# Kernel tuning notes

Hardware: AMD Instinct MI355X
Metric: run time of the kernel (lower is better)

Reference implementation:

```python
import jax, jax.numpy as jnp
import numpy as np

NODE_SIZE = 100000
DIM = 512
B = 2048
GAMMA = 3.0
LAMB = 20.0
TAU = 8.0


def setup_inputs() -> dict:
    key = jax.random.key(0)
    k1, k2 = jax.random.split(key)
    pairs = jax.random.randint(k1, (B, 2), 0, NODE_SIZE, dtype=jnp.int64 if jax.config.jax_enable_x64 else jnp.int32)
    emb = jax.random.normal(k2, (NODE_SIZE, DIM), dtype=jnp.float32)
    return {"pairs": pairs, "emb": emb}


def _align_loss(pairs, emb):
    l = pairs[:, 0]
    r = pairs[:, 1]
    l_emb = emb[l]                     # [B, D]
    r_emb = emb[r]                     # [B, D]
    pos_dis = jnp.sum(jnp.square(l_emb - r_emb), axis=-1, keepdims=True)  # [B, 1]

    emb_sq = jnp.sum(jnp.square(emb), axis=1)          # [N]

    def squared_dist(A):
        # ||a||^2 + ||b||^2 - 2 a.b  -> [B, N]
        a_sq = jnp.sum(jnp.square(A), axis=1, keepdims=True)
        return a_sq + emb_sq[None, :] - 2.0 * (A @ emb.T)

    l_neg_dis = squared_dist(l_emb)
    r_neg_dis = squared_dist(r_emb)

    # mask = 1 - one_hot(l) - one_hot(r), built without materializing one-hots
    rows = jnp.arange(B)
    mask = jnp.ones((B, NODE_SIZE), dtype=emb.dtype)
    mask = mask.at[rows, l].add(-1.0)
    mask = mask.at[rows, r].add(-1.0)

    def norm_lse(loss):
        loss = loss * mask
        mu = jax.lax.stop_gradient(jnp.mean(loss, axis=-1, keepdims=True))
        sd = jax.lax.stop_gradient(jnp.std(loss, axis=-1, keepdims=True))  # unbiased=False
        loss = (loss - mu) / sd
        return jax.scipy.special.logsumexp(LAMB * loss + TAU, axis=-1)

    l_loss = norm_lse(pos_dis - l_neg_dis + GAMMA)
    r_loss = norm_lse(pos_dis - r_neg_dis + GAMMA)
    return jnp.mean(l_loss + r_loss)


def reference(pairs, emb):
    return _align_loss(pairs, emb)
```

## Files before the change

### kernel.cpp

```cpp
#include <hip/hip_runtime.h>
#include <stdint.h>

#define NODES   100000
#define NPAD    100096
#define DIM     512
#define NPAIR   2048
#define MROWS   4096
#define NB      782
#define MPAGES  32
#define GAMMA_F 3.0f
#define LAMB_F  20.0f
#define TAU_F   8.0f
#define SHIFT_F 140.0f

#define TM 128
#define TN 128
#define BK 64

typedef __attribute__((ext_vector_type(8))) short          short8;
typedef __attribute__((ext_vector_type(8))) unsigned short ushort8;
typedef __attribute__((ext_vector_type(4))) float          f32x4;


__device__ __forceinline__ unsigned short f2bf(float f) {
    unsigned u = __float_as_uint(f);
    u += 0x7FFFu + ((u >> 16) & 1u);
    return (unsigned short)(u >> 16);
}
__device__ __forceinline__ float bf2f(unsigned short h) {
    return __uint_as_float(((unsigned)h) << 16);
}

__device__ __forceinline__ void gload_lds16(const void* g, void* l) {
    unsigned lofs = (unsigned)__builtin_amdgcn_readfirstlane((unsigned)(uintptr_t)l);
    auto lp = reinterpret_cast<__attribute__((address_space(3))) unsigned*>(lofs);
    auto gp = (const __attribute__((address_space(1))) unsigned*)g;
    __builtin_amdgcn_global_load_lds(gp, lp, 16, 0, 0);
}


__global__ void convert_stats_kernel(const float* __restrict__ emb,
                                     unsigned short* __restrict__ Ebf,
                                     float* __restrict__ esq,
                                     float* __restrict__ Spart,
                                     float* __restrict__ Tpart,
                                     float* __restrict__ E1part,
                                     float* __restrict__ E2part) {
    __shared__ float Sl[4][512];
    __shared__ float Tl[4][512];
    __shared__ float ew[8];
    const int b = blockIdx.x, t = threadIdx.x;
    const int lane = t & 63, wave = t >> 6;
    const int r0 = b * 196;
    float sacc[8], tacc[8];
    #pragma unroll
    for (int k = 0; k < 8; ++k) { sacc[k] = 0.f; tacc[k] = 0.f; }
    float e1 = 0.f, e2 = 0.f;
    for (int i = 0; i < 49; ++i) {
        const int row = r0 + i * 4 + wave;
        if (row >= NPAD) continue;
        const bool real = row < NODES;
        float v[8];
        float ss = 0.f;
        if (real) {
            const float4* p = (const float4*)(emb + (size_t)row * DIM + lane * 8);
            float4 a = p[0], bb = p[1];
            v[0]=a.x; v[1]=a.y; v[2]=a.z; v[3]=a.w;
            v[4]=bb.x; v[5]=bb.y; v[6]=bb.z; v[7]=bb.w;
            #pragma unroll
            for (int k = 0; k < 8; ++k) ss += v[k] * v[k];
        } else {
            #pragma unroll
            for (int k = 0; k < 8; ++k) v[k] = 0.f;
        }
        #pragma unroll
        for (int o = 1; o < 64; o <<= 1) ss += __shfl_xor(ss, o);
        ushort8 o8;
        float vr[8];
        #pragma unroll
        for (int k = 0; k < 8; ++k) { o8[k] = f2bf(v[k]); vr[k] = bf2f(o8[k]); }
        *(ushort8*)(Ebf + (size_t)row * DIM + lane * 8) = o8;
        if (lane == 0) esq[row] = ss;
        if (real) {
            #pragma unroll
            for (int k = 0; k < 8; ++k) { sacc[k] += vr[k]; tacc[k] += ss * vr[k]; }
            if (lane == 0) { e1 += ss; e2 += ss * ss; }
        }
    }
    #pragma unroll
    for (int k = 0; k < 8; ++k) {
        Sl[wave][lane * 8 + k] = sacc[k];
        Tl[wave][lane * 8 + k] = tacc[k];
    }
    if (lane == 0) { ew[wave] = e1; ew[4 + wave] = e2; }
    __syncthreads();
    #pragma unroll
    for (int kk = 0; kk < 2; ++kk) {
        const int d = 2 * t + kk;
        Spart[(size_t)b * 512 + d] = Sl[0][d] + Sl[1][d] + Sl[2][d] + Sl[3][d];
        Tpart[(size_t)b * 512 + d] = Tl[0][d] + Tl[1][d] + Tl[2][d] + Tl[3][d];
    }
    if (t == 0) E1part[b] = ew[0] + ew[1] + ew[2] + ew[3];
    if (t == 1) E2part[b] = ew[4] + ew[5] + ew[6] + ew[7];
}

__global__ void stats_merge_kernel(const float* __restrict__ Spart,
                                   const float* __restrict__ Tpart,
                                   const float* __restrict__ E1part,
                                   const float* __restrict__ E2part,
                                   float* __restrict__ Svec,
                                   float* __restrict__ Tvec,
                                   double* __restrict__ E12) {
    const int t = threadIdx.x;
    if (t < 512) {
        float s = 0.f;
        for (int b = 0; b < 512; ++b) s += Spart[(size_t)b * 512 + t];
        Svec[t] = s;
    } else {
        const int d = t - 512;
        float s = 0.f;
        for (int b = 0; b < 512; ++b) s += Tpart[(size_t)b * 512 + d];
        Tvec[d] = s;
    }
    if (t == 0) { double a = 0.0; for (int b = 0; b < 512; ++b) a += (double)E1part[b]; E12[0] = a; }
    if (t == 1) { double a = 0.0; for (int b = 0; b < 512; ++b) a += (double)E2part[b]; E12[1] = a; }
}

__global__ void gather_kernel(const int* __restrict__ pairs,
                              const float* __restrict__ emb,
                              unsigned short* __restrict__ Abf,
                              float* __restrict__ cvec,
                              float* __restrict__ posv) {
    const int p    = blockIdx.x;
    const int lane = threadIdx.x;
    const int li = pairs[2 * p], ri = pairs[2 * p + 1];
    const float4* pl = (const float4*)(emb + (size_t)li * DIM + lane * 8);
    const float4* pr = (const float4*)(emb + (size_t)ri * DIM + lane * 8);
    float4 a0 = pl[0], a1 = pl[1];
    float4 b0 = pr[0], b1 = pr[1];
    float la[8] = {a0.x,a0.y,a0.z,a0.w,a1.x,a1.y,a1.z,a1.w};
    float lb[8] = {b0.x,b0.y,b0.z,b0.w,b1.x,b1.y,b1.z,b1.w};
    float sa = 0.f, sb = 0.f, sd = 0.f;
    ushort8 oa, ob;
    #pragma unroll
    for (int i = 0; i < 8; ++i) {
        sa += la[i] * la[i];
        sb += lb[i] * lb[i];
        float d = la[i] - lb[i];
        sd += d * d;
        oa[i] = f2bf(la[i]);
        ob[i] = f2bf(lb[i]);
    }
    *(ushort8*)(Abf + (size_t)p * DIM + lane * 8)            = oa;
    *(ushort8*)(Abf + (size_t)(NPAIR + p) * DIM + lane * 8)  = ob;
    #pragma unroll
    for (int off = 1; off < 64; off <<= 1) {
        sa += __shfl_xor(sa, off);
        sb += __shfl_xor(sb, off);
        sd += __shfl_xor(sd, off);
    }
    if (lane == 0) {
        cvec[p]         = sd - sa + GAMMA_F;
        cvec[NPAIR + p] = sd - sb + GAMMA_F;
        posv[p]         = sd;
    }
}


__launch_bounds__(256, 2)
__global__ void gram_kernel(const unsigned short* __restrict__ Ebf,
                            float* __restrict__ Gpart) {
    __shared__ unsigned short ldsA[64 * 128];
    __shared__ unsigned short ldsB[64 * 128];
    const int tid  = threadIdx.x;
    const int lane = tid & 63;
    const int wave = tid >> 6;
    const int wx = wave & 1, wy = wave >> 1;
    const int d1base = blockIdx.y * 128;
    const int d2base = blockIdx.x * 128;
    const int bz = blockIdx.z;
    const int r15 = lane & 15, q = lane >> 4;

    f32x4 zero4 = {0.f, 0.f, 0.f, 0.f};
    f32x4 acc[4][4];
    #pragma unroll
    for (int i = 0; i < 4; ++i)
        #pragma unroll
        for (int j = 0; j < 4; ++j) acc[i][j] = zero4;

    for (int jc = bz; jc < NPAD / 64; jc += 32) {
        const int j0 = jc * 64;
        #pragma unroll
        for (int ii = 0; ii < 4; ++ii) {
            const int iss = wave * 4 + ii;
            const int row = iss * 4 + (lane >> 4);
            gload_lds16(Ebf + (size_t)(j0 + row) * DIM + d1base + (lane & 15) * 8,
                        &ldsA[iss * 4 * 128]);
            gload_lds16(Ebf + (size_t)(j0 + row) * DIM + d2base + (lane & 15) * 8,
                        &ldsB[iss * 4 * 128]);
        }
        __builtin_amdgcn_s_waitcnt(0);
        __syncthreads();
        #pragma unroll
        for (int h = 0; h < 2; ++h) {
            short8 af[4], bfv[4];
            #pragma unroll
            for (int mt = 0; mt < 4; ++mt) {
                const int m = wy * 64 + mt * 16 + r15;
                #pragma unroll
                for (int i = 0; i < 8; ++i)
                    af[mt][i] = (short)ldsA[(h * 32 + q * 8 + i) * 128 + m];
            }
            #pragma unroll
            for (int nt = 0; nt < 4; ++nt) {
                const int n = wx * 64 + nt * 16 + r15;
                #pragma unroll
                for (int i = 0; i < 8; ++i)
                    bfv[nt][i] = (short)ldsB[(h * 32 + q * 8 + i) * 128 + n];
            }
            #pragma unroll
            for (int mt = 0; mt < 4; ++mt)
                #pragma unroll
                for (int nt = 0; nt < 4; ++nt)
                    acc[mt][nt] = __builtin_amdgcn_mfma_f32_16x16x32_bf16(
                        af[mt], bfv[nt], acc[mt][nt], 0, 0, 0);
        }
        __syncthreads();
    }
    float* gp = Gpart + (size_t)bz * 512 * 512;
    #pragma unroll
    for (int mt = 0; mt < 4; ++mt)
        #pragma unroll
        for (int r = 0; r < 4; ++r) {
            const int d1 = d1base + wy * 64 + mt * 16 + q * 4 + r;
            #pragma unroll
            for (int nt = 0; nt < 4; ++nt) {
                const int d2 = d2base + wx * 64 + nt * 16 + r15;
                gp[d1 * 512 + d2] = acc[mt][nt][r];
            }
        }
}

__global__ void gram_merge_kernel(const float* __restrict__ Gpart,
                                  float* __restrict__ G) {
    const int idx = blockIdx.x * 256 + threadIdx.x;
    float s = 0.f;
    for (int b = 0; b < 32; ++b) s += Gpart[(size_t)b * 512 * 512 + idx];
    G[idx] = s;
}


__launch_bounds__(256)
__global__ void gu_kernel(const unsigned short* __restrict__ Abf,
                          const float* __restrict__ G,
                          const float* __restrict__ Svec,
                          const float* __restrict__ Tvec,
                          const double* __restrict__ E12,
                          const float* __restrict__ cvec,
                          const float* __restrict__ posv,
                          const int* __restrict__ pairs,
                          float* __restrict__ alpha_v,
                          float* __restrict__ shift_v) {
    __shared__ float u[8][512];
    __shared__ float red[8][3][4];
    const int t = threadIdx.x;
    const int lane = t & 63, wave = t >> 6;
    const int r0 = blockIdx.x * 8;
    #pragma unroll
    for (int p = 0; p < 8; ++p) {
        unsigned pk = *(const unsigned*)(Abf + (size_t)(r0 + p) * DIM + 2 * t);
        u[p][2 * t]     = bf2f((unsigned short)(pk & 0xffffu));
        u[p][2 * t + 1] = bf2f((unsigned short)(pk >> 16));
    }
    __syncthreads();
    float acc0[8], acc1[8];
    #pragma unroll
    for (int p = 0; p < 8; ++p) { acc0[p] = 0.f; acc1[p] = 0.f; }
    for (int d1 = 0; d1 < 512; ++d1) {
        const float2 g = *(const float2*)(G + d1 * 512 + 2 * t);
        #pragma unroll
        for (int p = 0; p < 8; ++p) {
            const float up = u[p][d1];
            acc0[p] += up * g.x;
            acc1[p] += up * g.y;
        }
    }
    const float sv0 = Svec[2 * t], sv1 = Svec[2 * t + 1];
    const float tv0 = Tvec[2 * t], tv1 = Tvec[2 * t + 1];
    #pragma unroll
    for (int p = 0; p < 8; ++p) {
        const float u0 = u[p][2 * t], u1 = u[p][2 * t + 1];
        float pdS = u0 * sv0 + u1 * sv1;
        float pdT = u0 * tv0 + u1 * tv1;
        float pq  = u0 * acc0[p] + u1 * acc1[p];
        #pragma unroll
        for (int off = 1; off < 64; off <<= 1) {
            pdS += __shfl_xor(pdS, off);
            pdT += __shfl_xor(pdT, off);
            pq  += __shfl_xor(pq,  off);
        }
        if (lane == 0) {
            red[p][0][wave] = pdS;
            red[p][1][wave] = pdT;
            red[p][2][wave] = pq;
        }
    }
    __syncthreads();
    if (t < 8) {
        const int p = t;
        const double dS = (double)red[p][0][0] + red[p][0][1] + red[p][0][2] + red[p][0][3];
        const double dT = (double)red[p][1][0] + red[p][1][1] + red[p][1][2] + red[p][1][3];
        const double qq = (double)red[p][2][0] + red[p][2][1] + red[p][2][2] + red[p][2][3];
        const int row = r0 + p;
        const int pp  = row & (NPAIR - 1);
        const double c  = (double)cvec[row];
        const double E1 = E12[0], E2 = E12[1];
        const double N  = (double)NODES;
        double Sx  = N * c + 2.0 * dS - E1;
        double Sxx = (N * c * c - 2.0 * c * E1 + E2) + 4.0 * (c * dS - dT) + 4.0 * qq;
        const int li = pairs[2 * pp], ri = pairs[2 * pp + 1];
        const double pos = (double)posv[pp];
        if (li != ri) {
            const double x1 = pos + (double)GAMMA_F, x2 = (double)GAMMA_F;
            Sx  -= x1 + x2;
            Sxx -= x1 * x1 + x2 * x2;
        } else {
            Sx -= 2.0 * (double)GAMMA_F;
        }
        const double mu  = Sx / N;
        const double var = Sxx / N - mu * mu;
        const double sd  = sqrt(fmax(var, 1e-30));
        const double al  = (double)LAMB_F / sd;
        alpha_v[row] = (float)al;
        shift_v[row] = (float)(al * mu + (double)SHIFT_F);
    }
}


__launch_bounds__(256, 2)
__global__ void gemm_kernel(const unsigned short* __restrict__ Abf,
                            const unsigned short* __restrict__ Ebf,
                            const float* __restrict__ cvec,
                            const float* __restrict__ esq,
                            const int*   __restrict__ pairs,
                            const float* __restrict__ alpha_v,
                            const float* __restrict__ shift_v,
                            float* __restrict__ psum) {
    __shared__ unsigned short ldsA[TM * BK];
    __shared__ unsigned short ldsB[TN * BK];
    __shared__ float red_s[2][TM];
    __shared__ float alsh[TM], csh[TM], cmsh[TM];
    __shared__ int   lish[TM], rish[TM];

    const int tid  = threadIdx.x;
    const int lane = tid & 63;
    const int wave = tid >> 6;
    const int wx = wave & 1;
    const int wy = wave >> 1;
    const int nb = blockIdx.x;
    const int n0 = nb * TN;
    const int m0 = blockIdx.y * TM;

    if (tid < TM) {
        const int gm = m0 + tid;
        alsh[tid] = alpha_v[gm];
        csh[tid]  = shift_v[gm];
        cmsh[tid] = cvec[gm];
        const int p = gm & (NPAIR - 1);
        lish[tid] = pairs[2 * p];
        rish[tid] = pairs[2 * p + 1];
    }

    f32x4 zero4 = {0.f, 0.f, 0.f, 0.f};
    f32x4 acc[4][4];
    #pragma unroll
    for (int i = 0; i < 4; ++i)
        #pragma unroll
        for (int j = 0; j < 4; ++j) acc[i][j] = zero4;

    const int lrow   = lane >> 3;
    const int lchunk = lane & 7;
    const int r15 = lane & 15;
    const int q   = lane >> 4;

    for (int kt = 0; kt < DIM / BK; ++kt) {
        const int kb = kt * BK;
        #pragma unroll
        for (int j = 0; j < 4; ++j) {
            const int rbase = (wave * 4 + j) * 8;
            const int row   = rbase + lrow;
            const int gch   = lchunk ^ (row & 7);
            gload_lds16(Abf + ((size_t)(m0 + row) * DIM + kb + gch * 8), &ldsA[rbase * BK]);
            gload_lds16(Ebf + ((size_t)(n0 + row) * DIM + kb + gch * 8), &ldsB[rbase * BK]);
        }
        __builtin_amdgcn_s_waitcnt(0);
        __syncthreads();
        #pragma unroll
        for (int h = 0; h < 2; ++h) {
            short8 af[4], bfr[4];
            #pragma unroll
            for (int mt = 0; mt < 4; ++mt) {
                int row = wy * 64 + mt * 16 + r15;
                int c   = (h * 4 + q) ^ (row & 7);
                af[mt] = *(const short8*)&ldsA[row * BK + c * 8];
            }
            #pragma unroll
            for (int nt = 0; nt < 4; ++nt) {
                int row = wx * 64 + nt * 16 + r15;
                int c   = (h * 4 + q) ^ (row & 7);
                bfr[nt] = *(const short8*)&ldsB[row * BK + c * 8];
            }
            #pragma unroll
            for (int mt = 0; mt < 4; ++mt)
                #pragma unroll
                for (int nt = 0; nt < 4; ++nt)
                    acc[mt][nt] = __builtin_amdgcn_mfma_f32_16x16x32_bf16(
                        af[mt], bfr[nt], acc[mt][nt], 0, 0, 0);
        }
        __syncthreads();
    }

    #pragma unroll
    for (int mt = 0; mt < 4; ++mt) {
        #pragma unroll
        for (int r = 0; r < 4; ++r) {
            const int rit = wy * 64 + mt * 16 + q * 4 + r;
            const float cm = cmsh[rit];
            const float al = alsh[rit];
            const float Cc = csh[rit];
            const int li = lish[rit], ri = rish[rit];
            float se = 0.f;
            #pragma unroll
            for (int nt = 0; nt < 4; ++nt) {
                const int gn = n0 + wx * 64 + nt * 16 + r15;
                float xv = cm + 2.0f * acc[mt][nt][r] - esq[gn];
                float msk = 1.0f - (float)(gn == li) - (float)(gn == ri);
                xv *= msk;
                float term = __expf(fmaf(al, xv, -Cc));
                se += (gn < NODES) ? term : 0.f;
            }
            #pragma unroll
            for (int o = 1; o < 16; o <<= 1) se += __shfl_xor(se, o);
            if (r15 == 0) red_s[wx][rit] = se;
        }
    }
    __syncthreads();
    if (tid < TM) {
        psum[(size_t)nb * MROWS + m0 + tid] = red_s[0][tid] + red_s[1][tid];
    }
}


__global__ void lse_part_kernel(const float* __restrict__ psum,
                                float* __restrict__ lsep) {
    const int row = blockIdx.x * 256 + threadIdx.x;
    const int c   = blockIdx.y;
    const int nb0 = c * 196;
    const int nb1 = (nb0 + 196 < NB) ? nb0 + 196 : NB;
    float s = 0.f;
    for (int nb = nb0; nb < nb1; ++nb)
        s += psum[(size_t)nb * MROWS + row];
    lsep[(size_t)c * MROWS + row] = s;
}

__global__ void loss_kernel(const float* __restrict__ lsep,
                            float* __restrict__ loss_v) {
    const int row = blockIdx.x * 256 + threadIdx.x;
    const float s = lsep[row] + lsep[MROWS + row]
                  + lsep[2 * MROWS + row] + lsep[3 * MROWS + row];
    loss_v[row] = (TAU_F + SHIFT_F) + logf(s);
}

__global__ void final_kernel(const float* __restrict__ loss_v,
                             float* __restrict__ out) {
    __shared__ double wpart[4];
    int t = threadIdx.x;
    double s = 0.0;
    for (int i = t; i < MROWS; i += 256)
        s += (double)loss_v[i];
    #pragma unroll
    for (int off = 1; off < 64; off <<= 1) s += __shfl_xor(s, off);
    if ((t & 63) == 0) wpart[t >> 6] = s;
    __syncthreads();
    if (t == 0) out[0] = (float)((wpart[0] + wpart[1] + wpart[2] + wpart[3]) / (double)NPAIR);
}


extern "C" void kernel_launch(void* const* d_in, const int* in_sizes, int n_in,
                              void* d_out, int out_size, void* d_ws, size_t ws_size,
                              hipStream_t stream) {
    const int*   pairs = (const int*)d_in[0];
    const float* emb   = (const float*)d_in[1];
    float* out = (float*)d_out;

    char* ws = (char*)d_ws;
    size_t off = 0;
    auto alloc = [&](size_t bytes) -> void* {
        void* p = ws + off;
        off += (bytes + 255) & ~(size_t)255;
        return p;
    };
    unsigned short* Ebf = (unsigned short*)alloc((size_t)NPAD * DIM * 2);
    unsigned short* Abf = (unsigned short*)alloc((size_t)MROWS * DIM * 2);
    float*  esq     = (float*)alloc((size_t)NPAD * 4);
    float*  cvec    = (float*)alloc((size_t)MROWS * 4);
    float*  posv    = (float*)alloc((size_t)NPAIR * 4);
    float*  Spart   = (float*)alloc((size_t)512 * DIM * 4);
    float*  Tpart   = (float*)alloc((size_t)512 * DIM * 4);
    float*  E1part  = (float*)alloc((size_t)512 * 4);
    float*  E2part  = (float*)alloc((size_t)512 * 4);
    float*  Svec    = (float*)alloc((size_t)DIM * 4);
    float*  Tvec    = (float*)alloc((size_t)DIM * 4);
    double* E12     = (double*)alloc(2 * sizeof(double));
    float*  G       = (float*)alloc((size_t)512 * 512 * 4);
    float*  alpha_v = (float*)alloc((size_t)MROWS * 4);
    float*  shift_v = (float*)alloc((size_t)MROWS * 4);
    float*  lsep    = (float*)alloc((size_t)4 * MROWS * 4);
    float*  loss_v  = (float*)alloc((size_t)MROWS * 4);
    char* uni = (char*)alloc((size_t)32 * 512 * 512 * 4);
    float* Gpart = (float*)uni;
    float* psum  = (float*)uni;
    if (off > ws_size) return;

    convert_stats_kernel<<<512, 256, 0, stream>>>(emb, Ebf, esq,
                                                  Spart, Tpart, E1part, E2part);
    stats_merge_kernel<<<1, 1024, 0, stream>>>(Spart, Tpart, E1part, E2part,
                                               Svec, Tvec, E12);
    gather_kernel<<<NPAIR, 64, 0, stream>>>(pairs, emb, Abf, cvec, posv);

    gram_kernel<<<dim3(4, 4, 32), 256, 0, stream>>>(Ebf, Gpart);
    gram_merge_kernel<<<1024, 256, 0, stream>>>(Gpart, G);
    gu_kernel<<<MROWS / 8, 256, 0, stream>>>(Abf, G, Svec, Tvec, E12,
                                             cvec, posv, pairs, alpha_v, shift_v);

    gemm_kernel<<<dim3(NB, MPAGES), 256, 0, stream>>>(Abf, Ebf, cvec, esq, pairs,
                                                      alpha_v, shift_v, psum);
    lse_part_kernel<<<dim3(16, 4), 256, 0, stream>>>(psum, lsep);
    loss_kernel<<<16, 256, 0, stream>>>(lsep, loss_v);
    final_kernel<<<1, 256, 0, stream>>>(loss_v, out);
}
```

Measured before the change: 1.109 ms.

## Parallelize stats merge, pad gram LDS, remap GEMM blocks, fuse LSE reductions

```diff
diff --git a/kernel.cpp b/kernel.cpp
--- a/kernel.cpp
+++ b/kernel.cpp
@@ -7,7 +7,6 @@
 #define NPAIR   2048
 #define MROWS   4096
 #define NB      782
-#define MPAGES  32
 #define GAMMA_F 3.0f
 #define LAMB_F  20.0f
 #define TAU_F   8.0f
@@ -111,19 +110,34 @@
                                    float* __restrict__ Svec,
                                    float* __restrict__ Tvec,
                                    double* __restrict__ E12) {
-    const int t = threadIdx.x;
-    if (t < 512) {
+    const int bid = blockIdx.x, t = threadIdx.x;
+    if (bid < 32) {
+        __shared__ float part[8][32];
+        const int col = (bid & 15) * 32 + (t & 31);
+        const int seg = t >> 5;
+        const float* src = (bid < 16) ? Spart : Tpart;
         float s = 0.f;
-        for (int b = 0; b < 512; ++b) s += Spart[(size_t)b * 512 + t];
-        Svec[t] = s;
+        const int b0 = seg * 64;
+        for (int b = b0; b < b0 + 64; ++b) s += src[(size_t)b * 512 + col];
+        part[seg][t & 31] = s;
+        __syncthreads();
+        if (t < 32) {
+            float r = 0.f;
+            #pragma unroll
+            for (int g = 0; g < 8; ++g) r += part[g][t];
+            const int c2 = (bid & 15) * 32 + t;
+            if (bid < 16) Svec[c2] = r; else Tvec[c2] = r;
+        }
     } else {
-        const int d = t - 512;
-        float s = 0.f;
-        for (int b = 0; b < 512; ++b) s += Tpart[(size_t)b * 512 + d];
-        Tvec[d] = s;
-    }
-    if (t == 0) { double a = 0.0; for (int b = 0; b < 512; ++b) a += (double)E1part[b]; E12[0] = a; }
-    if (t == 1) { double a = 0.0; for (int b = 0; b < 512; ++b) a += (double)E2part[b]; E12[1] = a; }
+        __shared__ double w[4];
+        const float* src = (bid == 32) ? E1part : E2part;
+        double s = (double)src[t] + (double)src[t + 256];
+        #pragma unroll
+        for (int o = 1; o < 64; o <<= 1) s += __shfl_xor(s, o);
+        if ((t & 63) == 0) w[t >> 6] = s;
+        __syncthreads();
+        if (t == 0) E12[bid - 32] = w[0] + w[1] + w[2] + w[3];
+    }
 }
 
 __global__ void gather_kernel(const int* __restrict__ pairs,
@@ -167,11 +181,13 @@
 }
 
 
+#define GPAD 520
+
 __launch_bounds__(256, 2)
 __global__ void gram_kernel(const unsigned short* __restrict__ Ebf,
                             float* __restrict__ Gpart) {
-    __shared__ unsigned short ldsA[64 * 128];
-    __shared__ unsigned short ldsB[64 * 128];
+    __shared__ unsigned short ldsA[16 * GPAD];
+    __shared__ unsigned short ldsB[16 * GPAD];
     const int tid  = threadIdx.x;
     const int lane = tid & 63;
     const int wave = tid >> 6;
@@ -195,9 +211,9 @@
             const int iss = wave * 4 + ii;
             const int row = iss * 4 + (lane >> 4);
             gload_lds16(Ebf + (size_t)(j0 + row) * DIM + d1base + (lane & 15) * 8,
-                        &ldsA[iss * 4 * 128]);
+                        &ldsA[iss * GPAD]);
             gload_lds16(Ebf + (size_t)(j0 + row) * DIM + d2base + (lane & 15) * 8,
-                        &ldsB[iss * 4 * 128]);
+                        &ldsB[iss * GPAD]);
         }
         __builtin_amdgcn_s_waitcnt(0);
         __syncthreads();
@@ -208,15 +224,19 @@
             for (int mt = 0; mt < 4; ++mt) {
                 const int m = wy * 64 + mt * 16 + r15;
                 #pragma unroll
-                for (int i = 0; i < 8; ++i)
-                    af[mt][i] = (short)ldsA[(h * 32 + q * 8 + i) * 128 + m];
+                for (int i = 0; i < 8; ++i) {
+                    const int r = h * 32 + q * 8 + i;
+                    af[mt][i] = (short)ldsA[(r >> 2) * GPAD + (r & 3) * 128 + m];
+                }
             }
             #pragma unroll
             for (int nt = 0; nt < 4; ++nt) {
                 const int n = wx * 64 + nt * 16 + r15;
                 #pragma unroll
-                for (int i = 0; i < 8; ++i)
-                    bfv[nt][i] = (short)ldsB[(h * 32 + q * 8 + i) * 128 + n];
+                for (int i = 0; i < 8; ++i) {
+                    const int r = h * 32 + q * 8 + i;
+                    bfv[nt][i] = (short)ldsB[(r >> 2) * GPAD + (r & 3) * 128 + n];
+                }
             }
             #pragma unroll
             for (int mt = 0; mt < 4; ++mt)
@@ -357,117 +377,121 @@
     const int wave = tid >> 6;
     const int wx = wave & 1;
     const int wy = wave >> 1;
-    const int nb = blockIdx.x;
-    const int n0 = nb * TN;
-    const int m0 = blockIdx.y * TM;
-
-    if (tid < TM) {
-        const int gm = m0 + tid;
-        alsh[tid] = alpha_v[gm];
-        csh[tid]  = shift_v[gm];
-        cmsh[tid] = cvec[gm];
-        const int p = gm & (NPAIR - 1);
-        lish[tid] = pairs[2 * p];
-        rish[tid] = pairs[2 * p + 1];
-    }
-
-    f32x4 zero4 = {0.f, 0.f, 0.f, 0.f};
-    f32x4 acc[4][4];
-    #pragma unroll
-    for (int i = 0; i < 4; ++i)
-        #pragma unroll
-        for (int j = 0; j < 4; ++j) acc[i][j] = zero4;
+
+    const int d = blockIdx.x;
+    const int j = (d & 7) * 782 + (d >> 3);
+    const int nb  = j >> 3;
+    const int mpg = j & 7;
+    const int n0  = nb * TN;
 
     const int lrow   = lane >> 3;
     const int lchunk = lane & 7;
     const int r15 = lane & 15;
     const int q   = lane >> 4;
 
-    for (int kt = 0; kt < DIM / BK; ++kt) {
-        const int kb = kt * BK;
-        #pragma unroll
-        for (int j = 0; j < 4; ++j) {
-            const int rbase = (wave * 4 + j) * 8;
-            const int row   = rbase + lrow;
-            const int gch   = lchunk ^ (row & 7);
-            gload_lds16(Abf + ((size_t)(m0 + row) * DIM + kb + gch * 8), &ldsA[rbase * BK]);
-            gload_lds16(Ebf + ((size_t)(n0 + row) * DIM + kb + gch * 8), &ldsB[rbase * BK]);
-        }
-        __builtin_amdgcn_s_waitcnt(0);
+    float eqv[4];
+    int   gnv[4];
+    #pragma unroll
+    for (int nt = 0; nt < 4; ++nt) {
+        const int gn = n0 + wx * 64 + nt * 16 + r15;
+        gnv[nt] = gn;
+        eqv[nt] = esq[gn];
+    }
+
+    for (int pg = 0; pg < 4; ++pg) {
+        const int m0 = (mpg * 4 + pg) * TM;
+
+        if (tid < TM) {
+            const int gm = m0 + tid;
+            alsh[tid] = alpha_v[gm];
+            csh[tid]  = shift_v[gm];
+            cmsh[tid] = cvec[gm];
+            const int p = gm & (NPAIR - 1);
+            lish[tid] = pairs[2 * p];
+            rish[tid] = pairs[2 * p + 1];
+        }
+
+        f32x4 zero4 = {0.f, 0.f, 0.f, 0.f};
+        f32x4 acc[4][4];
+        #pragma unroll
+        for (int i = 0; i < 4; ++i)
+            #pragma unroll
+            for (int jj = 0; jj < 4; ++jj) acc[i][jj] = zero4;
+
+        for (int kt = 0; kt < DIM / BK; ++kt) {
+            const int kb = kt * BK;
+            #pragma unroll
+            for (int jj = 0; jj < 4; ++jj) {
+                const int rbase = (wave * 4 + jj) * 8;
+                const int row   = rbase + lrow;
+                const int gch   = lchunk ^ (row & 7);
+                gload_lds16(Abf + ((size_t)(m0 + row) * DIM + kb + gch * 8), &ldsA[rbase * BK]);
+                gload_lds16(Ebf + ((size_t)(n0 + row) * DIM + kb + gch * 8), &ldsB[rbase * BK]);
+            }
+            __builtin_amdgcn_s_waitcnt(0);
+            __syncthreads();
+            #pragma unroll
+            for (int h = 0; h < 2; ++h) {
+                short8 af[4], bfr[4];
+                #pragma unroll
+                for (int mt = 0; mt < 4; ++mt) {
+                    int row = wy * 64 + mt * 16 + r15;
+                    int c   = (h * 4 + q) ^ (row & 7);
+                    af[mt] = *(const short8*)&ldsA[row * BK + c * 8];
+                }
+                #pragma unroll
+                for (int nt = 0; nt < 4; ++nt) {
+                    int row = wx * 64 + nt * 16 + r15;
+                    int c   = (h * 4 + q) ^ (row & 7);
+                    bfr[nt] = *(const short8*)&ldsB[row * BK + c * 8];
+                }
+                #pragma unroll
+                for (int mt = 0; mt < 4; ++mt)
+                    #pragma unroll
+                    for (int nt = 0; nt < 4; ++nt)
+                        acc[mt][nt] = __builtin_amdgcn_mfma_f32_16x16x32_bf16(
+                            af[mt], bfr[nt], acc[mt][nt], 0, 0, 0);
+            }
+            __syncthreads();
+        }
+
+        #pragma unroll
+        for (int mt = 0; mt < 4; ++mt) {
+            #pragma unroll
+            for (int r = 0; r < 4; ++r) {
+                const int rit = wy * 64 + mt * 16 + q * 4 + r;
+                const float cm = cmsh[rit];
+                const float al = alsh[rit];
+                const float Cc = csh[rit];
+                const int li = lish[rit], ri = rish[rit];
+                float se = 0.f;
+                #pragma unroll
+                for (int nt = 0; nt < 4; ++nt) {
+                    float xv = cm + 2.0f * acc[mt][nt][r] - eqv[nt];
+                    float msk = 1.0f - (float)(gnv[nt] == li) - (float)(gnv[nt] == ri);
+                    xv *= msk;
+                    float term = __expf(fmaf(al, xv, -Cc));
+                    se += (gnv[nt] < NODES) ? term : 0.f;
+                }
+                #pragma unroll
+                for (int o = 1; o < 16; o <<= 1) se += __shfl_xor(se, o);
+                if (r15 == 0) red_s[wx][rit] = se;
+            }
+        }
         __syncthreads();
-        #pragma unroll
-        for (int h = 0; h < 2; ++h) {
-            short8 af[4], bfr[4];
-            #pragma unroll
-            for (int mt = 0; mt < 4; ++mt) {
-                int row = wy * 64 + mt * 16 + r15;
-                int c   = (h * 4 + q) ^ (row & 7);
-                af[mt] = *(const short8*)&ldsA[row * BK + c * 8];
-            }
-            #pragma unroll
-            for (int nt = 0; nt < 4; ++nt) {
-                int row = wx * 64 + nt * 16 + r15;
-                int c   = (h * 4 + q) ^ (row & 7);
-                bfr[nt] = *(const short8*)&ldsB[row * BK + c * 8];
-            }
-            #pragma unroll
-            for (int mt = 0; mt < 4; ++mt)
-                #pragma unroll
-                for (int nt = 0; nt < 4; ++nt)
-                    acc[mt][nt] = __builtin_amdgcn_mfma_f32_16x16x32_bf16(
-                        af[mt], bfr[nt], acc[mt][nt], 0, 0, 0);
-        }
-        __syncthreads();
-    }
-
-    #pragma unroll
-    for (int mt = 0; mt < 4; ++mt) {
-        #pragma unroll
-        for (int r = 0; r < 4; ++r) {
-            const int rit = wy * 64 + mt * 16 + q * 4 + r;
-            const float cm = cmsh[rit];
-            const float al = alsh[rit];
-            const float Cc = csh[rit];
-            const int li = lish[rit], ri = rish[rit];
-            float se = 0.f;
-            #pragma unroll
-            for (int nt = 0; nt < 4; ++nt) {
-                const int gn = n0 + wx * 64 + nt * 16 + r15;
-                float xv = cm + 2.0f * acc[mt][nt][r] - esq[gn];
-                float msk = 1.0f - (float)(gn == li) - (float)(gn == ri);
-                xv *= msk;
-                float term = __expf(fmaf(al, xv, -Cc));
-                se += (gn < NODES) ? term : 0.f;
-            }
-            #pragma unroll
-            for (int o = 1; o < 16; o <<= 1) se += __shfl_xor(se, o);
-            if (r15 == 0) red_s[wx][rit] = se;
-        }
-    }
-    __syncthreads();
-    if (tid < TM) {
-        psum[(size_t)nb * MROWS + m0 + tid] = red_s[0][tid] + red_s[1][tid];
-    }
-}
-
-
-__global__ void lse_part_kernel(const float* __restrict__ psum,
-                                float* __restrict__ lsep) {
+        if (tid < TM) {
+            psum[(size_t)nb * MROWS + m0 + tid] = red_s[0][tid] + red_s[1][tid];
+        }
+    }
+}
+
+
+__global__ void lse_loss_kernel(const float* __restrict__ psum,
+                                float* __restrict__ loss_v) {
     const int row = blockIdx.x * 256 + threadIdx.x;
-    const int c   = blockIdx.y;
-    const int nb0 = c * 196;
-    const int nb1 = (nb0 + 196 < NB) ? nb0 + 196 : NB;
     float s = 0.f;
-    for (int nb = nb0; nb < nb1; ++nb)
+    for (int nb = 0; nb < NB; ++nb)
         s += psum[(size_t)nb * MROWS + row];
-    lsep[(size_t)c * MROWS + row] = s;
-}
-
-__global__ void loss_kernel(const float* __restrict__ lsep,
-                            float* __restrict__ loss_v) {
-    const int row = blockIdx.x * 256 + threadIdx.x;
-    const float s = lsep[row] + lsep[MROWS + row]
-                  + lsep[2 * MROWS + row] + lsep[3 * MROWS + row];
     loss_v[row] = (TAU_F + SHIFT_F) + logf(s);
 }
 
@@ -515,7 +539,6 @@
     float*  G       = (float*)alloc((size_t)512 * 512 * 4);
     float*  alpha_v = (float*)alloc((size_t)MROWS * 4);
     float*  shift_v = (float*)alloc((size_t)MROWS * 4);
-    float*  lsep    = (float*)alloc((size_t)4 * MROWS * 4);
     float*  loss_v  = (float*)alloc((size_t)MROWS * 4);
     char* uni = (char*)alloc((size_t)32 * 512 * 512 * 4);
     float* Gpart = (float*)uni;
@@ -524,7 +547,7 @@
 
     convert_stats_kernel<<<512, 256, 0, stream>>>(emb, Ebf, esq,
                                                   Spart, Tpart, E1part, E2part);
-    stats_merge_kernel<<<1, 1024, 0, stream>>>(Spart, Tpart, E1part, E2part,
+    stats_merge_kernel<<<34, 256, 0, stream>>>(Spart, Tpart, E1part, E2part,
                                                Svec, Tvec, E12);
     gather_kernel<<<NPAIR, 64, 0, stream>>>(pairs, emb, Abf, cvec, posv);
 
@@ -533,9 +556,8 @@
     gu_kernel<<<MROWS / 8, 256, 0, stream>>>(Abf, G, Svec, Tvec, E12,
                                              cvec, posv, pairs, alpha_v, shift_v);
 
-    gemm_kernel<<<dim3(NB, MPAGES), 256, 0, stream>>>(Abf, Ebf, cvec, esq, pairs,
-                                                      alpha_v, shift_v, psum);
-    lse_part_kernel<<<dim3(16, 4), 256, 0, stream>>>(psum, lsep);
-    loss_kernel<<<16, 256, 0, stream>>>(lsep, loss_v);
+    gemm_kernel<<<6256, 256, 0, stream>>>(Abf, Ebf, cvec, esq, pairs,
+                                          alpha_v, shift_v, psum);
+    lse_loss_kernel<<<16, 256, 0, stream>>>(psum, loss_v);
     final_kernel<<<1, 256, 0, stream>>>(loss_v, out);
 }
```

Result: no change. 1.093 ms (-1.4%).
